# Optimization experiments

Hardware: AMD Instinct MI355X
Metric: run time of the kernel (lower is better)

## Reference

```python
import jax, jax.numpy as jnp
import numpy as np

EMBED_DIM = 384
N_DOCS = 262144
BATCH = 64
TOP_K = 8
EPS = 1e-8


def setup_inputs() -> dict:
    key = jax.random.key(0)
    kq, kd = jax.random.split(key)
    query = jax.random.normal(kq, (BATCH, EMBED_DIM), dtype=jnp.float32)
    doc_embeddings = jax.random.normal(kd, (N_DOCS, EMBED_DIM), dtype=jnp.float32)
    return {"query": query, "doc_embeddings": doc_embeddings, "top_k": TOP_K}


def reference(query, doc_embeddings, top_k):
    # Cosine similarity: L2-normalize both sides.
    qn = query / (jnp.linalg.norm(query, axis=-1, keepdims=True) + EPS)          # [B, d]
    dn = doc_embeddings / (jnp.linalg.norm(doc_embeddings, axis=-1, keepdims=True) + EPS)  # [N, d]
    # Similarity scores between every query and every document.
    scores = jnp.einsum('bd,nd->bn', qn, dn)                                      # [B, N]
    # Top-k retrieval.
    topk_scores, topk_idx = jax.lax.top_k(scores, top_k)                          # [B, k]
    # Gather retrieved document embeddings.
    retrieved = dn[topk_idx]                                                      # [B, k, d]
    # Context fusion: softmax-weighted sum of retrieved docs.
    weights = jax.nn.softmax(topk_scores, axis=-1)                                # [B, k]
    fused = jnp.einsum('bk,bkd->bd', weights, retrieved)                          # [B, d]
    return fused, topk_scores, topk_idx
```

## Files before the change

kernel.cpp:

```cpp
#include <hip/hip_runtime.h>
#include <math.h>


#define EMBED 384
#define NDOCS 262144
#define BATCH 64
#define TOPK 8
#define DBLK 256
#define NBLK (NDOCS / DBLK)
#define EPSN 1e-8f
#define SCW 260
#define LO_OFF 20480u
#define RN_OFF 66560

typedef __attribute__((ext_vector_type(8))) short bf16x8;
typedef __attribute__((ext_vector_type(4))) float f32x4;

#define INS8(s_, i_) do {                                                     \
    if ((s_) > ts[7] || ((s_) == ts[7] && (i_) < ti[7])) {                    \
        ts[7] = (s_); ti[7] = (i_);                                           \
        _Pragma("unroll")                                                     \
        for (int r_ = 7; r_ > 0; --r_) {                                      \
            bool sw_ = (ts[r_] > ts[r_-1]) ||                                 \
                       (ts[r_] == ts[r_-1] && ti[r_] < ti[r_-1]);             \
            float a_ = ts[r_-1]; int b_ = ti[r_-1];                           \
            ts[r_-1] = sw_ ? ts[r_] : a_;  ti[r_-1] = sw_ ? ti[r_] : b_;      \
            ts[r_]   = sw_ ? a_ : ts[r_];  ti[r_]   = sw_ ? b_ : ti[r_];      \
        }                                                                     \
    }                                                                         \
} while (0)

template<int OFF>
__device__ __forceinline__ int4 gload_s(unsigned voff, const void* sbase) {
    int4 r;
    asm volatile("global_load_dwordx4 %0, %1, %2 offset:%3"
                 : "=v"(r) : "v"(voff), "s"(sbase), "i"(OFF) : "memory");
    return r;
}

__device__ __forceinline__ int4 dsread16(unsigned a) {
    int4 r;
    asm volatile("ds_read_b128 %0, %1" : "=v"(r) : "v"(a) : "memory");
    return r;
}

#define SPB(F, H, O) {                                                        \
    unsigned u_ = __float_as_uint(F);                                         \
    H = (u_ + 0x7fffu + ((u_ >> 16) & 1u)) >> 16;                             \
    float r_ = (F) - __uint_as_float((H) << 16);                              \
    unsigned v_ = __float_as_uint(r_);                                        \
    O = (v_ + 0x7fffu + ((v_ >> 16) & 1u)) >> 16;                             \
}

#define SPLIT4(J) {                                                           \
    f32x4 f_ = *(f32x4*)&ld[J];                                               \
    nacc[J] = fmaf(f_[0], f_[0], fmaf(f_[1], f_[1],                           \
              fmaf(f_[2], f_[2], fmaf(f_[3], f_[3], nacc[J]))));              \
    unsigned h0_, h1_, h2_, h3_, o0_, o1_, o2_, o3_;                          \
    SPB(f_[0], h0_, o0_); SPB(f_[1], h1_, o1_);                               \
    SPB(f_[2], h2_, o2_); SPB(f_[3], h3_, o3_);                               \
    sh[J].x = (h0_ & 0xffffu) | (h1_ << 16);                                  \
    sh[J].y = (h2_ & 0xffffu) | (h3_ << 16);                                  \
    sl[J].x = (o0_ & 0xffffu) | (o1_ << 16);                                  \
    sl[J].y = (o2_ & 0xffffu) | (o3_ << 16);                                  \
}

__global__ void qprep_kernel(const float* __restrict__ q,
                             unsigned short* __restrict__ qh,
                             unsigned short* __restrict__ ql) {
    const int row = blockIdx.x;
    const int lane = threadIdx.x;
    float v[6];
    float s = 0.f;
#pragma unroll
    for (int i = 0; i < 6; ++i) {
        v[i] = q[row * EMBED + lane + 64 * i];
        s = fmaf(v[i], v[i], s);
    }
#pragma unroll
    for (int off = 32; off > 0; off >>= 1) s += __shfl_xor(s, off);
    float rinv = 1.0f / (sqrtf(s) + EPSN);
#pragma unroll
    for (int i = 0; i < 6; ++i) {
        float f = v[i] * rinv;
        unsigned h, lo;
        SPB(f, h, lo);
        qh[row * EMBED + lane + 64 * i] = (unsigned short)h;
        ql[row * EMBED + lane + 64 * i] = (unsigned short)lo;
    }
}

__global__ __launch_bounds__(256, 2) void score_topk_kernel(
        const float* __restrict__ docs,
        const unsigned short* __restrict__ qh,
        const unsigned short* __restrict__ ql,
        float* __restrict__ pscore, int* __restrict__ pidx) {
    __shared__ __align__(16) char smem[67584];
    float* S  = (float*)smem;
    float* RN = (float*)(smem + RN_OFF);

    const int tid = threadIdx.x;
    const int l   = tid & 63;
    const int wv  = tid >> 6;
    const int rowl = l & 15;
    const int ksub = l >> 4;
    const int d0 = blockIdx.x * DBLK;
    const unsigned bse = (unsigned)(uintptr_t)smem;

    f32x4 acc[16];
#pragma unroll
    for (int s = 0; s < 16; ++s) acc[s] = (f32x4){0.f, 0.f, 0.f, 0.f};
    float nacc[8];
#pragma unroll
    for (int j = 0; j < 8; ++j) nacc[j] = 0.f;

    int4 qf[12][2];
    {
        unsigned vq = (unsigned)((wv * 16 + rowl) * (EMBED * 2) + ksub * 16);
#pragma unroll
        for (int kb = 0; kb < 12; ++kb) {
            qf[kb][0] = gload_s<0>(vq, qh);
            qf[kb][1] = gload_s<0>(vq, ql);
            vq += 64;
        }
    }

    unsigned voff[8];
#pragma unroll
    for (int j = 0; j < 8; ++j)
        voff[j] = (unsigned)((d0 + wv * 64 + j * 8 + (l >> 3)) * 1536u)
                + (unsigned)((l & 7) * 16);

    int4 ld[8];
#pragma unroll
    for (int j = 0; j < 8; ++j) ld[j] = gload_s<0>(voff[j], docs);

    uint2 sh[8], sl[8];
    asm volatile("s_waitcnt vmcnt(0)" ::: "memory");
    __builtin_amdgcn_sched_barrier(0);
#pragma unroll
    for (int j = 0; j < 8; ++j) SPLIT4(j);

    const unsigned wbase = wv * 5120u + (unsigned)((l >> 3) * 80 + (l & 7) * 8);
    const unsigned rbase = (unsigned)(rowl * 80 + ksub * 16);

#define KITER(KB, LAST) {                                                      \
    __syncthreads();                                \
    _Pragma("unroll")                                                          \
    for (int j = 0; j < 8; ++j) {                                              \
        *(uint2*)(smem + wbase + j * 640u) = sh[j];                            \
        *(uint2*)(smem + LO_OFF + wbase + j * 640u) = sl[j];                   \
    }                                                                          \
    __syncthreads();                                        \
    if (!(LAST)) {                                                             \
        _Pragma("unroll")                                                      \
        for (int j = 0; j < 8; ++j)                                            \
            ld[j] = gload_s<((KB) + 1) * 128>(voff[j], docs);                  \
    }                                                                          \
    {                                                                          \
        int4 fh0, fl0, fh1, fl1;                                               \
        fh0 = dsread16(bse + rbase);                                           \
        fl0 = dsread16(bse + rbase + LO_OFF);                                  \
        _Pragma("unroll")                                                      \
        for (int s = 0; s < 16; ++s) {                                         \
            if (s < 15) {                                                      \
                fh1 = dsread16(bse + rbase + (unsigned)((s + 1) * 1280));      \
                fl1 = dsread16(bse + rbase + (unsigned)((s + 1) * 1280) + LO_OFF); \
                asm volatile("s_waitcnt lgkmcnt(2)" ::: "memory");             \
            } else {                                                           \
                asm volatile("s_waitcnt lgkmcnt(0)" ::: "memory");             \
            }                                                                  \
            __builtin_amdgcn_sched_barrier(0);                                 \
            bf16x8 bh = *(bf16x8*)&fh0, bl = *(bf16x8*)&fl0;                   \
            bf16x8 ah = *(bf16x8*)&qf[KB][0], al = *(bf16x8*)&qf[KB][1];       \
            acc[s] = __builtin_amdgcn_mfma_f32_16x16x32_bf16(ah, bh, acc[s], 0, 0, 0); \
            acc[s] = __builtin_amdgcn_mfma_f32_16x16x32_bf16(al, bh, acc[s], 0, 0, 0); \
            acc[s] = __builtin_amdgcn_mfma_f32_16x16x32_bf16(ah, bl, acc[s], 0, 0, 0); \
            fh0 = fh1; fl0 = fl1;                                              \
        }                                                                      \
    }                                                                          \
    if (!(LAST)) {                                                             \
        asm volatile("s_waitcnt vmcnt(0)" ::: "memory");                       \
        __builtin_amdgcn_sched_barrier(0);                                     \
        _Pragma("unroll")                                                      \
        for (int j = 0; j < 8; ++j) SPLIT4(j);                                 \
    }                                                                          \
}

    KITER(0, 0)  KITER(1, 0)  KITER(2, 0)  KITER(3, 0)
    KITER(4, 0)  KITER(5, 0)  KITER(6, 0)  KITER(7, 0)
    KITER(8, 0)  KITER(9, 0)  KITER(10, 0) KITER(11, 1)
#undef KITER

#pragma unroll
    for (int j = 0; j < 8; ++j) {
        float t = nacc[j];
        t += __shfl_xor(t, 1);
        t += __shfl_xor(t, 2);
        t += __shfl_xor(t, 4);
        if ((l & 7) == 0)
            RN[wv * 64 + j * 8 + (l >> 3)] = 1.0f / (sqrtf(t) + EPSN);
    }
    __syncthreads();

#pragma unroll
    for (int s = 0; s < 16; ++s) {
        float rn = RN[s * 16 + rowl];
#pragma unroll
        for (int jj = 0; jj < 4; ++jj)
            S[(wv * 16 + ksub * 4 + jj) * SCW + s * 16 + rowl] = acc[s][jj] * rn;
    }
    __syncthreads();

    float ts[8]; int ti[8];
#pragma unroll
    for (int r = 0; r < 8; ++r) { ts[r] = -3.402823466e38f; ti[r] = 0x7fffffff; }
    const int q = tid & 63, qa = tid >> 6;
    for (int ii = 0; ii < 64; ++ii) {
        int d = qa * 64 + ((ii + q) & 63);
        float sc = S[q * SCW + d];
        INS8(sc, d0 + d);
    }
    __syncthreads();
#pragma unroll
    for (int r = 0; r < 8; ++r) {
        S[(qa * 64 + q) * 8 + r] = ts[r];
        S[2048 + (qa * 64 + q) * 8 + r] = __int_as_float(ti[r]);
    }
    __syncthreads();
    if (tid < 64) {
#pragma unroll
        for (int r = 0; r < 8; ++r) { ts[r] = -3.402823466e38f; ti[r] = 0x7fffffff; }
        for (int a = 0; a < 4; ++a) {
#pragma unroll
            for (int r = 0; r < 8; ++r) {
                float s2 = S[(a * 64 + q) * 8 + r];
                int i2 = __float_as_int(S[2048 + (a * 64 + q) * 8 + r]);
                INS8(s2, i2);
            }
        }
        size_t o = ((size_t)q * NBLK + blockIdx.x) * TOPK;
        *(float4*)&pscore[o]     = make_float4(ts[0], ts[1], ts[2], ts[3]);
        *(float4*)&pscore[o + 4] = make_float4(ts[4], ts[5], ts[6], ts[7]);
        *(int4*)&pidx[o]     = make_int4(ti[0], ti[1], ti[2], ti[3]);
        *(int4*)&pidx[o + 4] = make_int4(ti[4], ti[5], ti[6], ti[7]);
    }
}

__global__ __launch_bounds__(256) void merge_a_kernel(
        const float* __restrict__ pscore, const int* __restrict__ pidx,
        float* __restrict__ cs, int* __restrict__ ci) {
    const int q = blockIdx.x >> 2;
    const int c = blockIdx.x & 3;
    const int tid = threadIdx.x;
    __shared__ float ls[2048];
    __shared__ int   li[2048];
    __shared__ float ls2[512];
    __shared__ int   li2[512];
    __shared__ float ls3[64];
    __shared__ int   li3[64];

    {
        size_t o = ((size_t)q * NBLK + c * 256 + tid) * TOPK;
        float4 s0 = *(const float4*)&pscore[o];
        float4 s1 = *(const float4*)&pscore[o + 4];
        int4 i0 = *(const int4*)&pidx[o];
        int4 i1 = *(const int4*)&pidx[o + 4];
        ls[tid * 8 + 0] = s0.x; ls[tid * 8 + 1] = s0.y;
        ls[tid * 8 + 2] = s0.z; ls[tid * 8 + 3] = s0.w;
        ls[tid * 8 + 4] = s1.x; ls[tid * 8 + 5] = s1.y;
        ls[tid * 8 + 6] = s1.z; ls[tid * 8 + 7] = s1.w;
        li[tid * 8 + 0] = i0.x; li[tid * 8 + 1] = i0.y;
        li[tid * 8 + 2] = i0.z; li[tid * 8 + 3] = i0.w;
        li[tid * 8 + 4] = i1.x; li[tid * 8 + 5] = i1.y;
        li[tid * 8 + 6] = i1.z; li[tid * 8 + 7] = i1.w;
    }
    __syncthreads();

    float ts[8]; int ti[8];
    if (tid < 64) {
#pragma unroll
        for (int r = 0; r < 8; ++r) { ts[r] = -3.402823466e38f; ti[r] = 0x7fffffff; }
        for (int e = 0; e < 32; ++e) {
            int k = tid + e * 64;
            float s = ls[k]; int gi = li[k];
            INS8(s, gi);
        }
#pragma unroll
        for (int r = 0; r < 8; ++r) { ls2[tid * 8 + r] = ts[r]; li2[tid * 8 + r] = ti[r]; }
    }
    __syncthreads();
    if (tid < 8) {
#pragma unroll
        for (int r = 0; r < 8; ++r) { ts[r] = -3.402823466e38f; ti[r] = 0x7fffffff; }
        for (int e = 0; e < 64; ++e) {
            int k = tid + e * 8;
            float s = ls2[k]; int gi = li2[k];
            INS8(s, gi);
        }
#pragma unroll
        for (int r = 0; r < 8; ++r) { ls3[tid * 8 + r] = ts[r]; li3[tid * 8 + r] = ti[r]; }
    }
    __syncthreads();
    if (tid == 0) {
#pragma unroll
        for (int r = 0; r < 8; ++r) { ts[r] = -3.402823466e38f; ti[r] = 0x7fffffff; }
        for (int e = 0; e < 64; ++e) {
            float s = ls3[e]; int gi = li3[e];
            INS8(s, gi);
        }
        size_t o = (size_t)(q * 4 + c) * TOPK;
#pragma unroll
        for (int r = 0; r < 8; ++r) { cs[o + r] = ts[r]; ci[o + r] = ti[r]; }
    }
}

__global__ __launch_bounds__(256) void merge_b_kernel(
        const float* __restrict__ docs, const float* __restrict__ cs,
        const int* __restrict__ ci, float* __restrict__ out) {
    const int q = blockIdx.x;
    const int tid = threadIdx.x;
    __shared__ int   fi[TOPK];
    __shared__ float wr[TOPK];

    if (tid == 0) {
        float ts[8]; int ti[8];
#pragma unroll
        for (int r = 0; r < 8; ++r) { ts[r] = -3.402823466e38f; ti[r] = 0x7fffffff; }
        for (int e = 0; e < 32; ++e) {
            float s = cs[q * 32 + e]; int gi = ci[q * 32 + e];
            INS8(s, gi);
        }
        float m = ts[0];
        float w[8]; float sum = 0.f;
#pragma unroll
        for (int r = 0; r < 8; ++r) { w[r] = expf(ts[r] - m); sum += w[r]; }
        float rs = 1.0f / sum;
#pragma unroll
        for (int r = 0; r < 8; ++r) {
            fi[r] = ti[r];
            wr[r] = w[r] * rs;
            out[BATCH * EMBED + q * TOPK + r] = ts[r];
            out[BATCH * EMBED + BATCH * TOPK + q * TOPK + r] = (float)ti[r];
        }
    }
    __syncthreads();

    int lane = tid & 63, wave = tid >> 6;
    for (int r = wave; r < TOPK; r += 4) {
        const float* dp = docs + (size_t)fi[r] * EMBED;
        float s = 0.f;
#pragma unroll
        for (int i = 0; i < 6; ++i) { float v = dp[lane + 64 * i]; s = fmaf(v, v, s); }
#pragma unroll
        for (int off = 32; off > 0; off >>= 1) s += __shfl_xor(s, off);
        if (lane == 0) wr[r] = wr[r] / (sqrtf(s) + EPSN);
    }
    __syncthreads();

    for (int dim = tid; dim < EMBED; dim += 256) {
        float a = 0.f;
#pragma unroll
        for (int r = 0; r < 8; ++r)
            a += wr[r] * docs[(size_t)fi[r] * EMBED + dim];
        out[q * EMBED + dim] = a;
    }
}

extern "C" void kernel_launch(void* const* d_in, const int* in_sizes, int n_in,
                              void* d_out, int out_size, void* d_ws, size_t ws_size,
                              hipStream_t stream) {
    const float* query = (const float*)d_in[0];
    const float* docs  = (const float*)d_in[1];
    float* out = (float*)d_out;

    char* ws = (char*)d_ws;
    unsigned short* qh = (unsigned short*)ws;
    unsigned short* ql = (unsigned short*)(ws + 49152);
    float* pscore = (float*)(ws + 98304);
    int*   pidx   = (int*)(ws + 98304 + (size_t)NBLK * BATCH * TOPK * 4);
    char*  ws3    = ws + 98304 + 2 * (size_t)NBLK * BATCH * TOPK * 4;
    float* cs     = (float*)ws3;
    int*   ci     = (int*)(ws3 + BATCH * 4 * TOPK * 4);

    qprep_kernel<<<64, 64, 0, stream>>>(query, qh, ql);
    score_topk_kernel<<<NBLK, 256, 0, stream>>>(docs, qh, ql, pscore, pidx);
    merge_a_kernel<<<BATCH * 4, 256, 0, stream>>>(pscore, pidx, cs, ci);
    merge_b_kernel<<<BATCH, 256, 0, stream>>>(docs, cs, ci, out);
}
```

Measured before the change: 237.6 us.

## Halve doc tile to 128 and stream query fragments per K-step

Halves the documents per block from 256 to 128 and widens each K-step to 64 columns, so there are six iterations instead of twelve. Shared memory per block shrinks to about 37 KB with a new LDS layout, which allows more resident blocks. The query hi/lo fragments are now loaded from global memory each iteration instead of being held in 48 registers, cutting register pressure at the cost of repeated small loads. The grid doubles, so the partial top-k buffer grows and merge_a/merge_b are adjusted for twice as many candidates.

```diff
diff --git a/kernel.cpp b/kernel.cpp
--- a/kernel.cpp
+++ b/kernel.cpp
@@ -6,12 +6,13 @@
 #define NDOCS 262144
 #define BATCH 64
 #define TOPK 8
-#define DBLK 256
+#define DBLK 128
 #define NBLK (NDOCS / DBLK)
 #define EPSN 1e-8f
-#define SCW 260
-#define LO_OFF 20480u
-#define RN_OFF 66560
+#define SCW 132
+#define PL_HI1 9216u
+#define PL_LO  18432u
+#define RN_OFF 36864
 
 typedef __attribute__((ext_vector_type(8))) short bf16x8;
 typedef __attribute__((ext_vector_type(4))) float f32x4;
@@ -52,17 +53,17 @@
     O = (v_ + 0x7fffu + ((v_ >> 16) & 1u)) >> 16;                             \
 }
 
-#define SPLIT4(J) {                                                           \
-    f32x4 f_ = *(f32x4*)&ld[J];                                               \
-    nacc[J] = fmaf(f_[0], f_[0], fmaf(f_[1], f_[1],                           \
-              fmaf(f_[2], f_[2], fmaf(f_[3], f_[3], nacc[J]))));              \
+#define SPLIT4(C) {                                                           \
+    f32x4 f_ = *(f32x4*)&ld[C];                                               \
+    nacc[C] = fmaf(f_[0], f_[0], fmaf(f_[1], f_[1],                           \
+              fmaf(f_[2], f_[2], fmaf(f_[3], f_[3], nacc[C]))));              \
     unsigned h0_, h1_, h2_, h3_, o0_, o1_, o2_, o3_;                          \
     SPB(f_[0], h0_, o0_); SPB(f_[1], h1_, o1_);                               \
     SPB(f_[2], h2_, o2_); SPB(f_[3], h3_, o3_);                               \
-    sh[J].x = (h0_ & 0xffffu) | (h1_ << 16);                                  \
-    sh[J].y = (h2_ & 0xffffu) | (h3_ << 16);                                  \
-    sl[J].x = (o0_ & 0xffffu) | (o1_ << 16);                                  \
-    sl[J].y = (o2_ & 0xffffu) | (o3_ << 16);                                  \
+    sh[C].x = (h0_ & 0xffffu) | (h1_ << 16);                                  \
+    sh[C].y = (h2_ & 0xffffu) | (h3_ << 16);                                  \
+    sl[C].x = (o0_ & 0xffffu) | (o1_ << 16);                                  \
+    sl[C].y = (o2_ & 0xffffu) | (o3_ << 16);                                  \
 }
 
 __global__ void qprep_kernel(const float* __restrict__ q,
@@ -95,87 +96,89 @@
         const unsigned short* __restrict__ qh,
         const unsigned short* __restrict__ ql,
         float* __restrict__ pscore, int* __restrict__ pidx) {
-    __shared__ __align__(16) char smem[67584];
+    __shared__ __align__(16) char smem[37376];
     float* S  = (float*)smem;
     float* RN = (float*)(smem + RN_OFF);
 
     const int tid = threadIdx.x;
     const int l   = tid & 63;
     const int wv  = tid >> 6;
-    const int rowl = l & 15;
-    const int ksub = l >> 4;
     const int d0 = blockIdx.x * DBLK;
     const unsigned bse = (unsigned)(uintptr_t)smem;
 
-    f32x4 acc[16];
-#pragma unroll
-    for (int s = 0; s < 16; ++s) acc[s] = (f32x4){0.f, 0.f, 0.f, 0.f};
+    f32x4 acc[8];
+#pragma unroll
+    for (int s = 0; s < 8; ++s) acc[s] = (f32x4){0.f, 0.f, 0.f, 0.f};
     float nacc[8];
 #pragma unroll
-    for (int j = 0; j < 8; ++j) nacc[j] = 0.f;
-
-    int4 qf[12][2];
-    {
-        unsigned vq = (unsigned)((wv * 16 + rowl) * (EMBED * 2) + ksub * 16);
-#pragma unroll
-        for (int kb = 0; kb < 12; ++kb) {
-            qf[kb][0] = gload_s<0>(vq, qh);
-            qf[kb][1] = gload_s<0>(vq, ql);
-            vq += 64;
-        }
-    }
+    for (int c = 0; c < 8; ++c) nacc[c] = 0.f;
 
     unsigned voff[8];
 #pragma unroll
-    for (int j = 0; j < 8; ++j)
-        voff[j] = (unsigned)((d0 + wv * 64 + j * 8 + (l >> 3)) * 1536u)
-                + (unsigned)((l & 7) * 16);
+    for (int c = 0; c < 8; ++c)
+        voff[c] = (unsigned)((wv * 32 + 4 * c + (l >> 4)) * 1536)
+                + (unsigned)((l & 15) * 16);
+    const float* dblk = docs + (size_t)d0 * EMBED;
+
+    const unsigned voffq = (unsigned)((wv * 16 + (l & 15)) * (EMBED * 2)
+                                      + (l >> 4) * 16);
+
+    const unsigned whbase = ((unsigned)((l & 15) >> 3)) * PL_HI1
+                          + (unsigned)((wv * 32 + (l >> 4)) * 72 + (l & 7) * 8);
+    const unsigned rbase = (unsigned)((l & 15) * 72 + (l >> 4) * 16);
 
     int4 ld[8];
-#pragma unroll
-    for (int j = 0; j < 8; ++j) ld[j] = gload_s<0>(voff[j], docs);
-
     uint2 sh[8], sl[8];
+    int4 qf[2][2];
+
+#pragma unroll
+    for (int c = 0; c < 8; ++c) ld[c] = gload_s<0>(voff[c], dblk);
     asm volatile("s_waitcnt vmcnt(0)" ::: "memory");
     __builtin_amdgcn_sched_barrier(0);
 #pragma unroll
-    for (int j = 0; j < 8; ++j) SPLIT4(j);
-
-    const unsigned wbase = wv * 5120u + (unsigned)((l >> 3) * 80 + (l & 7) * 8);
-    const unsigned rbase = (unsigned)(rowl * 80 + ksub * 16);
-
-#define KITER(KB, LAST) {                                                      \
+    for (int c = 0; c < 8; ++c) SPLIT4(c);
+
+#define KITER(O, LAST) {                                                       \
     __syncthreads();                                \
     _Pragma("unroll")                                                          \
-    for (int j = 0; j < 8; ++j) {                                              \
-        *(uint2*)(smem + wbase + j * 640u) = sh[j];                            \
-        *(uint2*)(smem + LO_OFF + wbase + j * 640u) = sl[j];                   \
+    for (int c = 0; c < 8; ++c) {                                              \
+        *(uint2*)(smem + whbase + 288u * c) = sh[c];                           \
+        *(uint2*)(smem + PL_LO + whbase + 288u * c) = sl[c];                   \
     }                                                                          \
-    __syncthreads();                                        \
+    __syncthreads();                                         \
+    qf[0][0] = gload_s<(O) * 128>(voffq, qh);                                  \
+    qf[0][1] = gload_s<(O) * 128>(voffq, ql);                                  \
+    qf[1][0] = gload_s<(O) * 128 + 64>(voffq, qh);                             \
+    qf[1][1] = gload_s<(O) * 128 + 64>(voffq, ql);                             \
     if (!(LAST)) {                                                             \
         _Pragma("unroll")                                                      \
-        for (int j = 0; j < 8; ++j)                                            \
-            ld[j] = gload_s<((KB) + 1) * 128>(voff[j], docs);                  \
+        for (int c = 0; c < 8; ++c)                                            \
+            ld[c] = gload_s<((O) + 1) * 256>(voff[c], dblk);                   \
     }                                                                          \
+    asm volatile("s_waitcnt vmcnt(%0)" :: "i"((LAST) ? 0 : 8) : "memory");     \
+    __builtin_amdgcn_sched_barrier(0);                                         \
     {                                                                          \
         int4 fh0, fl0, fh1, fl1;                                               \
         fh0 = dsread16(bse + rbase);                                           \
-        fl0 = dsread16(bse + rbase + LO_OFF);                                  \
+        fl0 = dsread16(bse + rbase + PL_LO);                                   \
         _Pragma("unroll")                                                      \
-        for (int s = 0; s < 16; ++s) {                                         \
-            if (s < 15) {                                                      \
-                fh1 = dsread16(bse + rbase + (unsigned)((s + 1) * 1280));      \
-                fl1 = dsread16(bse + rbase + (unsigned)((s + 1) * 1280) + LO_OFF); \
+        for (int i = 0; i < 16; ++i) {                                         \
+            if (i < 15) {                                                      \
+                unsigned na = bse + (unsigned)(((i + 1) >> 3) * 9216)          \
+                            + (unsigned)(((i + 1) & 7) * 16 * 72) + rbase;     \
+                fh1 = dsread16(na);                                            \
+                fl1 = dsread16(na + PL_LO);                                    \
                 asm volatile("s_waitcnt lgkmcnt(2)" ::: "memory");             \
             } else {                                                           \
                 asm volatile("s_waitcnt lgkmcnt(0)" ::: "memory");             \
             }                                                                  \
             __builtin_amdgcn_sched_barrier(0);                                 \
             bf16x8 bh = *(bf16x8*)&fh0, bl = *(bf16x8*)&fl0;                   \
-            bf16x8 ah = *(bf16x8*)&qf[KB][0], al = *(bf16x8*)&qf[KB][1];       \
-            acc[s] = __builtin_amdgcn_mfma_f32_16x16x32_bf16(ah, bh, acc[s], 0, 0, 0); \
-            acc[s] = __builtin_amdgcn_mfma_f32_16x16x32_bf16(al, bh, acc[s], 0, 0, 0); \
-            acc[s] = __builtin_amdgcn_mfma_f32_16x16x32_bf16(ah, bl, acc[s], 0, 0, 0); \
+            bf16x8 ah = *(bf16x8*)&qf[i >> 3][0];                              \
+            bf16x8 al = *(bf16x8*)&qf[i >> 3][1];                              \
+            acc[i & 7] = __builtin_amdgcn_mfma_f32_16x16x32_bf16(ah, bh, acc[i & 7], 0, 0, 0); \
+            acc[i & 7] = __builtin_amdgcn_mfma_f32_16x16x32_bf16(al, bh, acc[i & 7], 0, 0, 0); \
+            acc[i & 7] = __builtin_amdgcn_mfma_f32_16x16x32_bf16(ah, bl, acc[i & 7], 0, 0, 0); \
             fh0 = fh1; fl0 = fl1;                                              \
         }                                                                      \
     }                                                                          \
@@ -183,32 +186,31 @@
         asm volatile("s_waitcnt vmcnt(0)" ::: "memory");                       \
         __builtin_amdgcn_sched_barrier(0);                                     \
         _Pragma("unroll")                                                      \
-        for (int j = 0; j < 8; ++j) SPLIT4(j);                                 \
+        for (int c = 0; c < 8; ++c) SPLIT4(c);                                 \
     }                                                                          \
 }
 
-    KITER(0, 0)  KITER(1, 0)  KITER(2, 0)  KITER(3, 0)
-    KITER(4, 0)  KITER(5, 0)  KITER(6, 0)  KITER(7, 0)
-    KITER(8, 0)  KITER(9, 0)  KITER(10, 0) KITER(11, 1)
+    KITER(0, 0) KITER(1, 0) KITER(2, 0) KITER(3, 0) KITER(4, 0) KITER(5, 1)
 #undef KITER
 
 #pragma unroll
-    for (int j = 0; j < 8; ++j) {
-        float t = nacc[j];
+    for (int c = 0; c < 8; ++c) {
+        float t = nacc[c];
         t += __shfl_xor(t, 1);
         t += __shfl_xor(t, 2);
         t += __shfl_xor(t, 4);
-        if ((l & 7) == 0)
-            RN[wv * 64 + j * 8 + (l >> 3)] = 1.0f / (sqrtf(t) + EPSN);
-    }
-    __syncthreads();
-
-#pragma unroll
-    for (int s = 0; s < 16; ++s) {
-        float rn = RN[s * 16 + rowl];
-#pragma unroll
-        for (int jj = 0; jj < 4; ++jj)
-            S[(wv * 16 + ksub * 4 + jj) * SCW + s * 16 + rowl] = acc[s][jj] * rn;
+        t += __shfl_xor(t, 8);
+        if ((l & 15) == 0)
+            RN[wv * 32 + 4 * c + (l >> 4)] = 1.0f / (sqrtf(t) + EPSN);
+    }
+    __syncthreads();
+
+#pragma unroll
+    for (int s = 0; s < 8; ++s) {
+        float rn = RN[s * 16 + (l & 15)];
+#pragma unroll
+        for (int j = 0; j < 4; ++j)
+            S[(wv * 16 + (l >> 4) * 4 + j) * SCW + s * 16 + (l & 15)] = acc[s][j] * rn;
     }
     __syncthreads();
 
@@ -216,8 +218,8 @@
 #pragma unroll
     for (int r = 0; r < 8; ++r) { ts[r] = -3.402823466e38f; ti[r] = 0x7fffffff; }
     const int q = tid & 63, qa = tid >> 6;
-    for (int ii = 0; ii < 64; ++ii) {
-        int d = qa * 64 + ((ii + q) & 63);
+    for (int ii = 0; ii < 32; ++ii) {
+        int d = qa * 32 + ((ii + q) & 31);
         float sc = S[q * SCW + d];
         INS8(sc, d0 + d);
     }
@@ -250,8 +252,8 @@
 __global__ __launch_bounds__(256) void merge_a_kernel(
         const float* __restrict__ pscore, const int* __restrict__ pidx,
         float* __restrict__ cs, int* __restrict__ ci) {
-    const int q = blockIdx.x >> 2;
-    const int c = blockIdx.x & 3;
+    const int q = blockIdx.x >> 3;
+    const int c = blockIdx.x & 7;
     const int tid = threadIdx.x;
     __shared__ float ls[2048];
     __shared__ int   li[2048];
@@ -309,7 +311,7 @@
             float s = ls3[e]; int gi = li3[e];
             INS8(s, gi);
         }
-        size_t o = (size_t)(q * 4 + c) * TOPK;
+        size_t o = (size_t)(q * 8 + c) * TOPK;
 #pragma unroll
         for (int r = 0; r < 8; ++r) { cs[o + r] = ts[r]; ci[o + r] = ti[r]; }
     }
@@ -327,8 +329,8 @@
         float ts[8]; int ti[8];
 #pragma unroll
         for (int r = 0; r < 8; ++r) { ts[r] = -3.402823466e38f; ti[r] = 0x7fffffff; }
-        for (int e = 0; e < 32; ++e) {
-            float s = cs[q * 32 + e]; int gi = ci[q * 32 + e];
+        for (int e = 0; e < 64; ++e) {
+            float s = cs[q * 64 + e]; int gi = ci[q * 64 + e];
             INS8(s, gi);
         }
         float m = ts[0];
@@ -381,10 +383,10 @@
     int*   pidx   = (int*)(ws + 98304 + (size_t)NBLK * BATCH * TOPK * 4);
     char*  ws3    = ws + 98304 + 2 * (size_t)NBLK * BATCH * TOPK * 4;
     float* cs     = (float*)ws3;
-    int*   ci     = (int*)(ws3 + BATCH * 4 * TOPK * 4);
+    int*   ci     = (int*)(ws3 + BATCH * 8 * TOPK * 4);
 
     qprep_kernel<<<64, 64, 0, stream>>>(query, qh, ql);
     score_topk_kernel<<<NBLK, 256, 0, stream>>>(docs, qh, ql, pscore, pidx);
-    merge_a_kernel<<<BATCH * 4, 256, 0, stream>>>(pscore, pidx, cs, ci);
+    merge_a_kernel<<<BATCH * 8, 256, 0, stream>>>(pscore, pidx, cs, ci);
     merge_b_kernel<<<BATCH, 256, 0, stream>>>(docs, cs, ci, out);
 }
```

Result: slower. 330.0 us (+38.9%).
